# Kernel optimization log

Measured on AMD Instinct MI355X. Metric: run time of the kernel, lower is better.

Reference implementation:

```python
import jax, jax.numpy as jnp
import numpy as np

N = 50000
E = 400000
DIM_IN = 512
DIM_H = 64
HEADS = 8
DIM_OUT = 40
SLOPE = 0.2  # PyG GATv2Conv default negative_slope


def setup_inputs() -> dict:
    key = jax.random.key(0)
    ks = jax.random.split(key, 16)
    s = 0.05
    return {
        "x": jax.random.normal(ks[0], (N, DIM_IN), dtype=jnp.float32),
        "edge_index": jax.random.randint(ks[1], (2, E), 0, N, dtype=jnp.int64),
        "Wl1": jax.random.normal(ks[2], (DIM_IN, HEADS * DIM_H), dtype=jnp.float32) * s,
        "Wr1": jax.random.normal(ks[3], (DIM_IN, HEADS * DIM_H), dtype=jnp.float32) * s,
        "att1": jax.random.normal(ks[4], (HEADS, DIM_H), dtype=jnp.float32) * s,
        "b1": jax.random.normal(ks[5], (HEADS * DIM_H,), dtype=jnp.float32) * s,
        "Wl2": jax.random.normal(ks[6], (HEADS * DIM_H, DIM_OUT), dtype=jnp.float32) * s,
        "Wr2": jax.random.normal(ks[7], (HEADS * DIM_H, DIM_OUT), dtype=jnp.float32) * s,
        "att2": jax.random.normal(ks[8], (1, DIM_OUT), dtype=jnp.float32) * s,
        "b2": jax.random.normal(ks[9], (DIM_OUT,), dtype=jnp.float32) * s,
        "Wl3": jax.random.normal(ks[10], (HEADS * DIM_H, 2), dtype=jnp.float32) * s,
        "Wr3": jax.random.normal(ks[11], (HEADS * DIM_H, 2), dtype=jnp.float32) * s,
        "att3": jax.random.normal(ks[12], (1, 2), dtype=jnp.float32) * s,
        "b3": jax.random.normal(ks[13], (2,), dtype=jnp.float32) * s,
    }


def gatv2(x, src, dst, Wl, Wr, att, b):
    # PyG GATv2Conv: e_ij = att . LeakyReLU(W_l x_j + W_r x_i); softmax over j (by dst i);
    # out_i = sum_j alpha_ij * (W_l x_j); heads concatenated; bias added after.
    n = x.shape[0]
    H, F = att.shape
    xl = (x @ Wl).reshape(n, H, F)  # source transform
    xr = (x @ Wr).reshape(n, H, F)  # target transform
    e = jax.nn.leaky_relu(xl[src] + xr[dst], negative_slope=SLOPE)  # [E, H, F]
    logits = jnp.einsum("ehf,hf->eh", e, att)  # [E, H]
    m = jax.ops.segment_max(logits, dst, num_segments=n)  # self-loops => every segment nonempty
    ex = jnp.exp(logits - m[dst])
    denom = jax.ops.segment_sum(ex, dst, num_segments=n)
    alpha = ex / denom[dst]  # [E, H]
    out = jax.ops.segment_sum(xl[src] * alpha[:, :, None], dst, num_segments=n)  # [N, H, F]
    return out.reshape(n, H * F) + b


def reference(x, edge_index, Wl1, Wr1, att1, b1, Wl2, Wr2, att2, b2, Wl3, Wr3, att3, b3):
    # add self loops (PyG default add_self_loops=True)
    loops = jnp.arange(N, dtype=edge_index.dtype)
    ei = jnp.concatenate([edge_index, jnp.stack([loops, loops])], axis=1)
    src, dst = ei[0], ei[1]
    # eval mode: dropout is identity; ReverseLayerF is identity in forward
    h = jax.nn.relu(gatv2(x, src, dst, Wl1, Wr1, att1, b1))
    y_class = gatv2(h, src, dst, Wl2, Wr2, att2, b2)
    y_domain = gatv2(h, src, dst, Wl3, Wr3, att3, b3)
    return (y_class, y_domain)
```

## Files before the change

kernel.cpp:

```cpp
#include <hip/hip_runtime.h>
#include <math.h>

typedef unsigned short u16;
typedef unsigned int   u32;
typedef __attribute__((ext_vector_type(8))) short bf16x8;
typedef __attribute__((ext_vector_type(4))) float f32x4;
typedef __attribute__((ext_vector_type(4))) u32   u32x4;

__device__ __forceinline__ float b2f(u16 u) {
  union { u32 i; float f; } v; v.i = ((u32)u) << 16; return v.f;
}
__device__ __forceinline__ u16 f2b(float f) {
  union { u32 i; float f; } v; v.f = f;
  u32 r = v.i + 0x7FFFu + ((v.i >> 16) & 1u);
  return (u16)(r >> 16);
}
__device__ __forceinline__ float blo(u32 w) {
  union { u32 i; float f; } v; v.i = w << 16; return v.f;
}
__device__ __forceinline__ float bhi(u32 w) {
  union { u32 i; float f; } v; v.i = w & 0xFFFF0000u; return v.f;
}
__device__ __forceinline__ void ld_lds16(const u16* g, u16* l) {
  __builtin_amdgcn_global_load_lds((const __attribute__((address_space(1))) void*)g,
                                   (__attribute__((address_space(3))) void*)l, 16, 0, 0);
}

#define NN 50000
#define NE 400000
#define NT 450000
#define NBLK_SCAN 196

__global__ void k_detect(const void* x, const void* ei, int* flags) {
  __shared__ int cnt[2];
  int t = threadIdx.x;
  if (t < 2) cnt[t] = 0;
  __syncthreads();
  u16 u = ((const u16*)x)[t];
  int e = (u >> 7) & 0xFF;
  if (u == 0 || (e >= 90 && e <= 134)) atomicAdd(&cnt[0], 1);
  if (t < 16) {
    if (((const int*)ei)[2 * t + 1] == 0) atomicAdd(&cnt[1], 1);
  }
  __syncthreads();
  if (t == 0) {
    flags[0] = (cnt[0] >= 110) ? 1 : 0;
    flags[1] = (cnt[1] >= 15) ? 1 : 0;
  }
}

__device__ __forceinline__ int eidx(const int* ei, int pos, int i64) {
  return i64 ? ei[2 * pos] : ei[pos];
}

__global__ void k_convert_x(const void* x, const int* flags, u16* xb) {
  if (flags[0]) return;
  int c = blockIdx.x * 256 + threadIdx.x;
  const float* xf = (const float*)x + (size_t)c * 8;
  u32x4 o;
  #pragma unroll
  for (int i = 0; i < 4; ++i) {
    u32 lo = f2b(xf[2 * i]);
    u32 hi = f2b(xf[2 * i + 1]);
    o[i] = lo | (hi << 16);
  }
  *(u32x4*)(xb + (size_t)c * 8) = o;
}

__global__ void k_pack_w1t(const void* Wl1, const void* Wr1, const int* flags, u16* w1t) {
  int t = blockIdx.x * 256 + threadIdx.x;
  int k = t >> 10;
  int c = t & 1023;
  const void* W = (c < 512) ? Wl1 : Wr1;
  int cc = c & 511;
  u16 v;
  if (flags[0]) v = ((const u16*)W)[k * 512 + cc];
  else          v = f2b(((const float*)W)[k * 512 + cc]);
  w1t[c * 512 + k] = v;
}

__global__ void k_pack_w23t(const void* Wl2, const void* Wr2, const void* Wl3, const void* Wr3,
                            const int* flags, u16* w23t) {
  int t = blockIdx.x * 256 + threadIdx.x;
  int k = t / 96;
  int c = t % 96;
  const void* W = nullptr; int idx = 0;
  if (c < 40)      { W = Wl2; idx = k * 40 + c; }
  else if (c < 42) { W = Wl3; idx = k * 2 + (c - 40); }
  else if (c < 82) { W = Wr2; idx = k * 40 + (c - 42); }
  else if (c < 84) { W = Wr3; idx = k * 2 + (c - 82); }
  u16 v = 0;
  if (W) {
    if (flags[0]) v = ((const u16*)W)[idx];
    else          v = f2b(((const float*)W)[idx]);
  }
  w23t[c * 512 + k] = v;
}

__global__ void k_pack_params(const void* att1, const void* b1, const void* att2, const void* b2,
                              const void* att3, const void* b3, const int* flags, float* params) {
  int t = blockIdx.x * 256 + threadIdx.x;
  if (t >= 1108) return;
  const void* src; int idx;
  if (t < 512)       { src = att1; idx = t; }
  else if (t < 1024) { src = b1;   idx = t - 512; }
  else if (t < 1064) { src = att2; idx = t - 1024; }
  else if (t < 1104) { src = b2;   idx = t - 1064; }
  else if (t < 1106) { src = att3; idx = t - 1104; }
  else               { src = b3;   idx = t - 1106; }
  params[t] = flags[0] ? b2f(((const u16*)src)[idx]) : ((const float*)src)[idx];
}

__global__ void k_hist(const int* ei, const int* flags, int* deg) {
  int e = blockIdx.x * 256 + threadIdx.x;
  if (e >= NE) return;
  int d = eidx(ei, NE + e, flags[1]);
  atomicAdd(&deg[d], 1);
}

__global__ void k_scanA(const int* deg, int* row_ptr, int* bsum) {
  __shared__ int sh[256];
  int b = blockIdx.x, t = threadIdx.x;
  int i = b * 256 + t;
  int val = (i < NN) ? deg[i] + 1 : 0;
  sh[t] = val;
  __syncthreads();
  #pragma unroll
  for (int off = 1; off < 256; off <<= 1) {
    int v = (t >= off) ? sh[t - off] : 0;
    __syncthreads();
    sh[t] += v;
    __syncthreads();
  }
  if (i < NN) row_ptr[i] = sh[t] - val;
  if (t == 255) bsum[b] = sh[255];
}

__global__ void k_scanB(int* bsum, int* row_ptr) {
  __shared__ int sh[256];
  int t = threadIdx.x;
  int val = (t < NBLK_SCAN) ? bsum[t] : 0;
  sh[t] = val;
  __syncthreads();
  #pragma unroll
  for (int off = 1; off < 256; off <<= 1) {
    int v = (t >= off) ? sh[t - off] : 0;
    __syncthreads();
    sh[t] += v;
    __syncthreads();
  }
  if (t < NBLK_SCAN) bsum[t] = sh[t] - val;
  if (t == 255) row_ptr[NN] = sh[255];
}

__global__ void k_scanC(const int* bsum, int* row_ptr, int* cursor) {
  int i = blockIdx.x * 256 + threadIdx.x;
  if (i < NN) {
    int v = row_ptr[i] + bsum[blockIdx.x];
    row_ptr[i] = v;
    cursor[i] = v;
  }
}

__global__ void k_scatter(const int* ei, const int* flags, int* cursor, int* csr_src) {
  int t = blockIdx.x * 256 + threadIdx.x;
  if (t >= NT) return;
  int i64 = flags[1];
  int s, d;
  if (t < NE) { s = eidx(ei, t, i64); d = eidx(ei, NE + t, i64); }
  else        { s = d = t - NE; }
  int pos = atomicAdd(&cursor[d], 1);
  csr_src[pos] = s;
}

__global__ __launch_bounds__(256) void k_gemm1(const void* __restrict__ xraw, const u16* __restrict__ xb,
                                               const u16* __restrict__ Bt, const int* __restrict__ flags,
                                               u16* __restrict__ XL, u16* __restrict__ XR) {
  __shared__ __align__(16) u16 As[128 * 64];
  __shared__ __align__(16) u16 Bs[128 * 64];
  const int id  = blockIdx.x;
  const int xcd = id & 7;
  const int lb  = id >> 3;
  const int mt  = xcd * 49 + (lb >> 3);
  const int nt  = lb & 7;
  if (mt >= 391) return;
  const int m0 = mt * 128;
  const int n0 = nt * 128;
  const u16* __restrict__ A = flags[0] ? (const u16*)xraw : xb;
  const int t = threadIdx.x;
  const int wave = t >> 6;
  const int lane = t & 63;
  const int wm = (wave >> 1) * 64;
  const int wn = (wave & 1) * 64;
  const int fr = lane & 15;
  const int fk = lane >> 4;
  const int srow = lane >> 3;
  const int schk = (lane & 7) ^ srow;
  f32x4 acc[4][4] = {};
  for (int k0 = 0; k0 < 512; k0 += 64) {
    #pragma unroll
    for (int q = 0; q < 4; ++q) {
      int rbase = wave * 32 + q * 8;
      int gm = m0 + rbase + srow;
      if (gm > NN - 1) gm = NN - 1;
      ld_lds16(&A[(size_t)gm * 512 + k0 + schk * 8], &As[rbase * 64]);
      ld_lds16(&Bt[(size_t)(n0 + rbase + srow) * 512 + k0 + schk * 8], &Bs[rbase * 64]);
    }
    __syncthreads();
    #pragma unroll
    for (int h = 0; h < 2; ++h) {
      int s = h * 4 + fk;
      bf16x8 af[4], bb[4];
      #pragma unroll
      for (int i = 0; i < 4; ++i) {
        int row = wm + i * 16 + fr;
        af[i] = *(const bf16x8*)&As[row * 64 + ((s ^ (row & 7)) * 8)];
      }
      #pragma unroll
      for (int j = 0; j < 4; ++j) {
        int row = wn + j * 16 + fr;
        bb[j] = *(const bf16x8*)&Bs[row * 64 + ((s ^ (row & 7)) * 8)];
      }
      #pragma unroll
      for (int i = 0; i < 4; ++i)
        #pragma unroll
        for (int j = 0; j < 4; ++j)
          acc[i][j] = __builtin_amdgcn_mfma_f32_16x16x32_bf16(af[i], bb[j], acc[i][j], 0, 0, 0);
    }
    __syncthreads();
  }
  #pragma unroll
  for (int i = 0; i < 4; ++i) {
    #pragma unroll
    for (int r = 0; r < 4; ++r) {
      int gm = m0 + wm + i * 16 + fk * 4 + r;
      if (gm < NN) {
        #pragma unroll
        for (int j = 0; j < 4; ++j) {
          int gn = n0 + wn + j * 16 + fr;
          u16 v = f2b(acc[i][j][r]);
          if (gn < 512) XL[(size_t)gm * 512 + gn] = v;
          else          XR[(size_t)gm * 512 + gn - 512] = v;
        }
      }
    }
  }
}

__global__ __launch_bounds__(256) void k_gemm2(const u16* __restrict__ A, const u16* __restrict__ Bt,
                                               float* __restrict__ C) {
  __shared__ __align__(16) short As[128][40];
  __shared__ __align__(16) short Bs[96][40];
  const int m0 = blockIdx.x * 128;
  const int t = threadIdx.x;
  const int wave = t >> 6;
  const int lane = t & 63;
  const int fr = lane & 15;
  const int fk = lane >> 4;
  const int wm = wave * 32;
  f32x4 acc[2][6] = {};
  for (int k0 = 0; k0 < 512; k0 += 32) {
    #pragma unroll
    for (int h = 0; h < 2; ++h) {
      int c = t + h * 256;
      int row = c >> 2, kc = (c & 3) * 8;
      int gm = m0 + row;
      u32x4 va = {0, 0, 0, 0};
      if (gm < NN) va = *(const u32x4*)&A[(size_t)gm * 512 + k0 + kc];
      *(u32x4*)&As[row][kc] = va;
    }
    for (int c = t; c < 384; c += 256) {
      int row = c >> 2, kc = (c & 3) * 8;
      *(u32x4*)&Bs[row][kc] = *(const u32x4*)&Bt[row * 512 + k0 + kc];
    }
    __syncthreads();
    bf16x8 af[2], bb[6];
    #pragma unroll
    for (int i = 0; i < 2; ++i) af[i] = *(const bf16x8*)&As[wm + i * 16 + fr][fk * 8];
    #pragma unroll
    for (int j = 0; j < 6; ++j) bb[j] = *(const bf16x8*)&Bs[j * 16 + fr][fk * 8];
    #pragma unroll
    for (int i = 0; i < 2; ++i)
      #pragma unroll
      for (int j = 0; j < 6; ++j)
        acc[i][j] = __builtin_amdgcn_mfma_f32_16x16x32_bf16(af[i], bb[j], acc[i][j], 0, 0, 0);
    __syncthreads();
  }
  #pragma unroll
  for (int i = 0; i < 2; ++i) {
    #pragma unroll
    for (int j = 0; j < 6; ++j) {
      int gn = j * 16 + fr;
      if (gn < 84) {
        #pragma unroll
        for (int r = 0; r < 4; ++r) {
          int gm = m0 + wm + i * 16 + fk * 4 + r;
          if (gm < NN) C[(size_t)gm * 84 + gn] = acc[i][j][r];
        }
      }
    }
  }
}

__global__ __launch_bounds__(256) void k_layer1f(const u16* __restrict__ xl1, const u16* __restrict__ xr1,
                                                 const int* __restrict__ row_ptr, const int* __restrict__ csr_src,
                                                 const float* __restrict__ params, u16* __restrict__ hb) {
  int wid = blockIdx.x * 4 + (threadIdx.x >> 6);
  int lane = threadIdx.x & 63;
  int nw = gridDim.x * 4;
  float att[8];
  #pragma unroll
  for (int k = 0; k < 8; ++k) att[k] = params[lane * 8 + k];
  for (int i = wid; i < NN; i += nw) {
    int e0 = row_ptr[i], e1 = row_ptr[i + 1];
    u32x4 xrv = *(const u32x4*)&xr1[(size_t)i * 512 + lane * 8];
    float xr[8];
    #pragma unroll
    for (int q = 0; q < 4; ++q) { xr[2 * q] = blo(xrv[q]); xr[2 * q + 1] = bhi(xrv[q]); }
    float s = 0.f;
    float acc[8] = {0.f, 0.f, 0.f, 0.f, 0.f, 0.f, 0.f, 0.f};
    int q0 = csr_src[e0];
    int q1 = csr_src[e0 + 1 < e1 ? e0 + 1 : e1 - 1];
    int q2 = csr_src[e0 + 2 < e1 ? e0 + 2 : e1 - 1];
    int q3 = csr_src[e0 + 3 < e1 ? e0 + 3 : e1 - 1];
    for (int p = e0; p < e1; p += 4) {
      int j0 = q0, j1 = q1, j2 = q2, j3 = q3;
      u32x4 v0 = *(const u32x4*)&xl1[(size_t)j0 * 512 + lane * 8];
      u32x4 v1 = *(const u32x4*)&xl1[(size_t)j1 * 512 + lane * 8];
      u32x4 v2 = *(const u32x4*)&xl1[(size_t)j2 * 512 + lane * 8];
      u32x4 v3 = *(const u32x4*)&xl1[(size_t)j3 * 512 + lane * 8];
      int np = p + 4;
      if (np < e1) {
        q0 = csr_src[np];
        q1 = csr_src[np + 1 < e1 ? np + 1 : e1 - 1];
        q2 = csr_src[np + 2 < e1 ? np + 2 : e1 - 1];
        q3 = csr_src[np + 3 < e1 ? np + 3 : e1 - 1];
      }
      float m1 = (p + 1 < e1) ? 1.f : 0.f;
      float m2 = (p + 2 < e1) ? 1.f : 0.f;
      float m3 = (p + 3 < e1) ? 1.f : 0.f;
      float c0 = 0.f, c1 = 0.f, c2 = 0.f, c3 = 0.f;
      float xlv0[8], xlv1[8], xlv2[8], xlv3[8];
      #pragma unroll
      for (int q = 0; q < 4; ++q) {
        xlv0[2 * q] = blo(v0[q]); xlv0[2 * q + 1] = bhi(v0[q]);
        xlv1[2 * q] = blo(v1[q]); xlv1[2 * q + 1] = bhi(v1[q]);
        xlv2[2 * q] = blo(v2[q]); xlv2[2 * q + 1] = bhi(v2[q]);
        xlv3[2 * q] = blo(v3[q]); xlv3[2 * q + 1] = bhi(v3[q]);
      }
      #pragma unroll
      for (int k = 0; k < 8; ++k) {
        float t0 = xlv0[k] + xr[k];
        float t1 = xlv1[k] + xr[k];
        float t2 = xlv2[k] + xr[k];
        float t3 = xlv3[k] + xr[k];
        c0 = fmaf(att[k], fmaxf(t0, 0.2f * t0), c0);
        c1 = fmaf(att[k], fmaxf(t1, 0.2f * t1), c1);
        c2 = fmaf(att[k], fmaxf(t2, 0.2f * t2), c2);
        c3 = fmaf(att[k], fmaxf(t3, 0.2f * t3), c3);
      }
      c0 += __shfl_xor(c0, 1, 64); c1 += __shfl_xor(c1, 1, 64);
      c2 += __shfl_xor(c2, 1, 64); c3 += __shfl_xor(c3, 1, 64);
      c0 += __shfl_xor(c0, 2, 64); c1 += __shfl_xor(c1, 2, 64);
      c2 += __shfl_xor(c2, 2, 64); c3 += __shfl_xor(c3, 2, 64);
      c0 += __shfl_xor(c0, 4, 64); c1 += __shfl_xor(c1, 4, 64);
      c2 += __shfl_xor(c2, 4, 64); c3 += __shfl_xor(c3, 4, 64);
      float pv0 = __expf(fminf(fmaxf(c0, -30.f), 30.f));
      float pv1 = __expf(fminf(fmaxf(c1, -30.f), 30.f)) * m1;
      float pv2 = __expf(fminf(fmaxf(c2, -30.f), 30.f)) * m2;
      float pv3 = __expf(fminf(fmaxf(c3, -30.f), 30.f)) * m3;
      s += (pv0 + pv1) + (pv2 + pv3);
      #pragma unroll
      for (int k = 0; k < 8; ++k) {
        float a = fmaf(pv0, xlv0[k], pv1 * xlv1[k]);
        float b = fmaf(pv2, xlv2[k], pv3 * xlv3[k]);
        acc[k] += a + b;
      }
    }
    float r = 1.f / s;
    u32x4 o;
    #pragma unroll
    for (int q = 0; q < 4; ++q) {
      u32 lo = f2b(fmaxf(fmaf(acc[2 * q],     r, params[512 + lane * 8 + 2 * q]),     0.f));
      u32 hi = f2b(fmaxf(fmaf(acc[2 * q + 1], r, params[512 + lane * 8 + 2 * q + 1]), 0.f));
      o[q] = lo | (hi << 16);
    }
    *(u32x4*)&hb[(size_t)i * 512 + lane * 8] = o;
  }
}

__global__ __launch_bounds__(256) void k_layer23f(const float* __restrict__ xlr23, const int* __restrict__ row_ptr,
                                                  const int* __restrict__ csr_src, const float* __restrict__ params,
                                                  const int* __restrict__ flags, void* __restrict__ out) {
  int wid = blockIdx.x * 4 + (threadIdx.x >> 6);
  int lane = threadIdx.x & 63;
  int nw = gridDim.x * 4;
  int c = lane;
  bool act = c < 42;
  float att = 0.f;
  if (c < 40)      att = params[1024 + c];
  else if (c < 42) att = params[1104 + (c - 40)];
  int isbf = flags[0];
  for (int i = wid; i < NN; i += nw) {
    int e0 = row_ptr[i], e1 = row_ptr[i + 1];
    float xr = act ? xlr23[(size_t)i * 84 + 42 + c] : 0.f;
    float s2 = 0.f, s3 = 0.f, acc = 0.f;
    for (int p = e0; p < e1; p += 2) {
      int p1 = p + 1 < e1 ? p + 1 : e1 - 1;
      float m1 = (p + 1 < e1) ? 1.f : 0.f;
      int j0 = csr_src[p], j1 = csr_src[p1];
      float xl0 = act ? xlr23[(size_t)j0 * 84 + c] : 0.f;
      float xl1 = act ? xlr23[(size_t)j1 * 84 + c] : 0.f;
      float t0 = xl0 + xr, t1 = xl1 + xr;
      float v0 = att * fmaxf(t0, 0.2f * t0);
      float v1 = att * fmaxf(t1, 0.2f * t1);
      float w0 = (c < 40) ? v0 : 0.f;
      float w1 = (c < 40) ? v1 : 0.f;
      #pragma unroll
      for (int o = 32; o >= 1; o >>= 1) { w0 += __shfl_xor(w0, o, 64); w1 += __shfl_xor(w1, o, 64); }
      float u0 = v0 + __shfl_xor(v0, 1, 64);
      float u1 = v1 + __shfl_xor(v1, 1, 64);
      float l3_0 = __shfl(u0, 40, 64);
      float l3_1 = __shfl(u1, 40, 64);
      float p2_0 = __expf(fminf(fmaxf(w0, -30.f), 30.f));
      float p2_1 = __expf(fminf(fmaxf(w1, -30.f), 30.f)) * m1;
      float p3_0 = __expf(fminf(fmaxf(l3_0, -30.f), 30.f));
      float p3_1 = __expf(fminf(fmaxf(l3_1, -30.f), 30.f)) * m1;
      s2 += p2_0 + p2_1;
      s3 += p3_0 + p3_1;
      float a0 = (c < 40) ? p2_0 : p3_0;
      float a1 = (c < 40) ? p2_1 : p3_1;
      acc += fmaf(a0, xl0, a1 * xl1);
    }
    if (c < 40) {
      float v = acc / s2 + params[1064 + c];
      size_t o = (size_t)i * 40 + c;
      if (isbf) ((u16*)out)[o] = f2b(v); else ((float*)out)[o] = v;
    } else if (c < 42) {
      float v = acc / s3 + params[1106 + (c - 40)];
      size_t o = 2000000 + (size_t)i * 2 + (c - 40);
      if (isbf) ((u16*)out)[o] = f2b(v); else ((float*)out)[o] = v;
    }
  }
}

extern "C" void kernel_launch(void* const* d_in, const int* in_sizes, int n_in,
                              void* d_out, int out_size, void* d_ws, size_t ws_size,
                              hipStream_t stream) {
  const void* x    = d_in[0];
  const int*  ei   = (const int*)d_in[1];
  const void* Wl1  = d_in[2];
  const void* Wr1  = d_in[3];
  const void* att1 = d_in[4];
  const void* b1   = d_in[5];
  const void* Wl2  = d_in[6];
  const void* Wr2  = d_in[7];
  const void* att2 = d_in[8];
  const void* b2   = d_in[9];
  const void* Wl3  = d_in[10];
  const void* Wr3  = d_in[11];
  const void* att3 = d_in[12];
  const void* b3   = d_in[13];
  (void)in_sizes; (void)n_in; (void)out_size;

  char* ws = (char*)d_ws;
  size_t off = 0;
  auto alloc = [&](size_t bytes) -> void* {
    void* p = ws + off;
    off = (off + bytes + 255) & ~(size_t)255;
    return p;
  };
  int*   flags   = (int*)  alloc(64);
  u16*   xb      = (u16*)  alloc((size_t)NN * 512 * 2);
  u16*   w1t     = (u16*)  alloc((size_t)1024 * 512 * 2);
  u16*   xl1     = (u16*)  alloc((size_t)NN * 512 * 2);
  u16*   xr1     = (u16*)  alloc((size_t)NN * 512 * 2);
  u16*   hb      = (u16*)  alloc((size_t)NN * 512 * 2);
  u16*   w23t    = (u16*)  alloc((size_t)96 * 512 * 2);
  float* xlr23   = (float*)alloc((size_t)NN * 84 * 4);
  float* params  = (float*)alloc(1108 * 4);
  int*   row_ptr = (int*)  alloc((NN + 1) * 4);
  int*   deg     = (int*)  alloc(NN * 4);
  int*   cursor  = (int*)  alloc(NN * 4);
  int*   csr_src = (int*)  alloc((NT + 16) * 4);
  int*   bsum    = (int*)  alloc(256 * 4);
  if (ws_size < off) return;

  hipLaunchKernelGGL(k_detect, dim3(1), dim3(128), 0, stream, x, (const void*)ei, flags);
  hipLaunchKernelGGL(k_convert_x, dim3(12500), dim3(256), 0, stream, x, flags, xb);
  hipLaunchKernelGGL(k_pack_w1t, dim3(2048), dim3(256), 0, stream, Wl1, Wr1, flags, w1t);
  hipLaunchKernelGGL(k_pack_w23t, dim3(192), dim3(256), 0, stream, Wl2, Wr2, Wl3, Wr3, flags, w23t);
  hipLaunchKernelGGL(k_pack_params, dim3(5), dim3(256), 0, stream, att1, b1, att2, b2, att3, b3, flags, params);
  hipMemsetAsync(deg, 0, NN * 4, stream);
  hipLaunchKernelGGL(k_hist, dim3((NE + 255) / 256), dim3(256), 0, stream, ei, flags, deg);
  hipLaunchKernelGGL(k_scanA, dim3(NBLK_SCAN), dim3(256), 0, stream, deg, row_ptr, bsum);
  hipLaunchKernelGGL(k_scanB, dim3(1), dim3(256), 0, stream, bsum, row_ptr);
  hipLaunchKernelGGL(k_scanC, dim3(NBLK_SCAN), dim3(256), 0, stream, bsum, row_ptr, cursor);
  hipLaunchKernelGGL(k_scatter, dim3((NT + 255) / 256), dim3(256), 0, stream, ei, flags, cursor, csr_src);
  hipLaunchKernelGGL(k_gemm1, dim3(3136), dim3(256), 0, stream, x, xb, w1t, flags, xl1, xr1);
  hipLaunchKernelGGL(k_layer1f, dim3(4096), dim3(256), 0, stream, xl1, xr1, row_ptr, csr_src, params, hb);
  hipLaunchKernelGGL(k_gemm2, dim3(391), dim3(256), 0, stream, hb, w23t, xlr23);
  hipLaunchKernelGGL(k_layer23f, dim3(4096), dim3(256), 0, stream, xlr23, row_ptr, csr_src, params, flags, d_out);
}
```

Before: 471.8 us.

## Split LeakyReLU into linear plus abs term, precompute linear dots in GEMM epilogue

Rewrites LeakyReLU(t) as 0.6*t + 0.4*|t|, so the linear part of the attention logit becomes per-node dot products (att·xl_j and att·xr_i). The GEMM1 epilogue computes these per head and stores them in dotL/dotR. The edge loop then only needs fabs plus an FMA per element, and it adds the two precomputed scalars. The aggregation sums are also restructured into FMA chains. This trades a cheaper per-edge inner loop for an extra gathered scalar load per edge, extra epilogue shuffles in GEMM1, and bf16 rounding differences because the dot is taken from fp32 accumulators.

```diff
diff --git a/kernel.cpp b/kernel.cpp
--- a/kernel.cpp
+++ b/kernel.cpp
@@ -175,7 +175,9 @@
 
 __global__ __launch_bounds__(256) void k_gemm1(const void* __restrict__ xraw, const u16* __restrict__ xb,
                                                const u16* __restrict__ Bt, const int* __restrict__ flags,
-                                               u16* __restrict__ XL, u16* __restrict__ XR) {
+                                               const float* __restrict__ params,
+                                               u16* __restrict__ XL, u16* __restrict__ XR,
+                                               float* __restrict__ dotL, float* __restrict__ dotR) {
   __shared__ __align__(16) u16 As[128 * 64];
   __shared__ __align__(16) u16 Bs[128 * 64];
   const int id  = blockIdx.x;
@@ -229,6 +231,31 @@
     }
     __syncthreads();
   }
+  {
+    const int cb = (n0 + wn) & 511;
+    const bool isL = (n0 + wn) < 512;
+    const int hd = cb >> 6;
+    float* __restrict__ dvec = isL ? dotL : dotR;
+    float attv[4];
+    #pragma unroll
+    for (int j = 0; j < 4; ++j) attv[j] = params[cb + j * 16 + fr];
+    #pragma unroll
+    for (int i = 0; i < 4; ++i) {
+      #pragma unroll
+      for (int r = 0; r < 4; ++r) {
+        float d = attv[0] * acc[i][0][r];
+        d = fmaf(attv[1], acc[i][1][r], d);
+        d = fmaf(attv[2], acc[i][2][r], d);
+        d = fmaf(attv[3], acc[i][3][r], d);
+        d += __shfl_xor(d, 1, 64);
+        d += __shfl_xor(d, 2, 64);
+        d += __shfl_xor(d, 4, 64);
+        d += __shfl_xor(d, 8, 64);
+        int gm = m0 + wm + i * 16 + fk * 4 + r;
+        if (fr == 0 && gm < NN) dvec[(size_t)gm * 8 + hd] = 0.6f * d;
+      }
+    }
+  }
   #pragma unroll
   for (int i = 0; i < 4; ++i) {
     #pragma unroll
@@ -303,17 +330,20 @@
 }
 
 __global__ __launch_bounds__(256) void k_layer1f(const u16* __restrict__ xl1, const u16* __restrict__ xr1,
+                                                 const float* __restrict__ dotL, const float* __restrict__ dotR,
                                                  const int* __restrict__ row_ptr, const int* __restrict__ csr_src,
                                                  const float* __restrict__ params, u16* __restrict__ hb) {
   int wid = blockIdx.x * 4 + (threadIdx.x >> 6);
   int lane = threadIdx.x & 63;
   int nw = gridDim.x * 4;
+  int grp = lane >> 3;
   float att[8];
   #pragma unroll
-  for (int k = 0; k < 8; ++k) att[k] = params[lane * 8 + k];
+  for (int k = 0; k < 8; ++k) att[k] = 0.4f * params[lane * 8 + k];
   for (int i = wid; i < NN; i += nw) {
     int e0 = row_ptr[i], e1 = row_ptr[i + 1];
     u32x4 xrv = *(const u32x4*)&xr1[(size_t)i * 512 + lane * 8];
+    float dRi = dotR[(size_t)i * 8 + grp];
     float xr[8];
     #pragma unroll
     for (int q = 0; q < 4; ++q) { xr[2 * q] = blo(xrv[q]); xr[2 * q + 1] = bhi(xrv[q]); }
@@ -329,6 +359,10 @@
       u32x4 v1 = *(const u32x4*)&xl1[(size_t)j1 * 512 + lane * 8];
       u32x4 v2 = *(const u32x4*)&xl1[(size_t)j2 * 512 + lane * 8];
       u32x4 v3 = *(const u32x4*)&xl1[(size_t)j3 * 512 + lane * 8];
+      float dl0 = dotL[(size_t)j0 * 8 + grp];
+      float dl1 = dotL[(size_t)j1 * 8 + grp];
+      float dl2 = dotL[(size_t)j2 * 8 + grp];
+      float dl3 = dotL[(size_t)j3 * 8 + grp];
       int np = p + 4;
       if (np < e1) {
         q0 = csr_src[np];
@@ -354,10 +388,10 @@
         float t1 = xlv1[k] + xr[k];
         float t2 = xlv2[k] + xr[k];
         float t3 = xlv3[k] + xr[k];
-        c0 = fmaf(att[k], fmaxf(t0, 0.2f * t0), c0);
-        c1 = fmaf(att[k], fmaxf(t1, 0.2f * t1), c1);
-        c2 = fmaf(att[k], fmaxf(t2, 0.2f * t2), c2);
-        c3 = fmaf(att[k], fmaxf(t3, 0.2f * t3), c3);
+        c0 = fmaf(att[k], fabsf(t0), c0);
+        c1 = fmaf(att[k], fabsf(t1), c1);
+        c2 = fmaf(att[k], fabsf(t2), c2);
+        c3 = fmaf(att[k], fabsf(t3), c3);
       }
       c0 += __shfl_xor(c0, 1, 64); c1 += __shfl_xor(c1, 1, 64);
       c2 += __shfl_xor(c2, 1, 64); c3 += __shfl_xor(c3, 1, 64);
@@ -365,16 +399,21 @@
       c2 += __shfl_xor(c2, 2, 64); c3 += __shfl_xor(c3, 2, 64);
       c0 += __shfl_xor(c0, 4, 64); c1 += __shfl_xor(c1, 4, 64);
       c2 += __shfl_xor(c2, 4, 64); c3 += __shfl_xor(c3, 4, 64);
-      float pv0 = __expf(fminf(fmaxf(c0, -30.f), 30.f));
-      float pv1 = __expf(fminf(fmaxf(c1, -30.f), 30.f)) * m1;
-      float pv2 = __expf(fminf(fmaxf(c2, -30.f), 30.f)) * m2;
-      float pv3 = __expf(fminf(fmaxf(c3, -30.f), 30.f)) * m3;
+      float l0 = c0 + dl0 + dRi;
+      float l1 = c1 + dl1 + dRi;
+      float l2 = c2 + dl2 + dRi;
+      float l3 = c3 + dl3 + dRi;
+      float pv0 = __expf(fminf(fmaxf(l0, -30.f), 30.f));
+      float pv1 = __expf(fminf(fmaxf(l1, -30.f), 30.f)) * m1;
+      float pv2 = __expf(fminf(fmaxf(l2, -30.f), 30.f)) * m2;
+      float pv3 = __expf(fminf(fmaxf(l3, -30.f), 30.f)) * m3;
       s += (pv0 + pv1) + (pv2 + pv3);
       #pragma unroll
       for (int k = 0; k < 8; ++k) {
-        float a = fmaf(pv0, xlv0[k], pv1 * xlv1[k]);
-        float b = fmaf(pv2, xlv2[k], pv3 * xlv3[k]);
-        acc[k] += a + b;
+        float a = fmaf(pv0, xlv0[k], acc[k]);
+        a = fmaf(pv1, xlv1[k], a);
+        a = fmaf(pv2, xlv2[k], a);
+        acc[k] = fmaf(pv3, xlv3[k], a);
       }
     }
     float r = 1.f / s;
@@ -430,7 +469,7 @@
       s3 += p3_0 + p3_1;
       float a0 = (c < 40) ? p2_0 : p3_0;
       float a1 = (c < 40) ? p2_1 : p3_1;
-      acc += fmaf(a0, xl0, a1 * xl1);
+      acc = fmaf(a1, xl1, fmaf(a0, xl0, acc));
     }
     if (c < 40) {
       float v = acc / s2 + params[1064 + c];
@@ -479,6 +518,8 @@
   u16*   w23t    = (u16*)  alloc((size_t)96 * 512 * 2);
   float* xlr23   = (float*)alloc((size_t)NN * 84 * 4);
   float* params  = (float*)alloc(1108 * 4);
+  float* dotL    = (float*)alloc((size_t)NN * 8 * 4);
+  float* dotR    = (float*)alloc((size_t)NN * 8 * 4);
   int*   row_ptr = (int*)  alloc((NN + 1) * 4);
   int*   deg     = (int*)  alloc(NN * 4);
   int*   cursor  = (int*)  alloc(NN * 4);
@@ -497,8 +538,8 @@
   hipLaunchKernelGGL(k_scanB, dim3(1), dim3(256), 0, stream, bsum, row_ptr);
   hipLaunchKernelGGL(k_scanC, dim3(NBLK_SCAN), dim3(256), 0, stream, bsum, row_ptr, cursor);
   hipLaunchKernelGGL(k_scatter, dim3((NT + 255) / 256), dim3(256), 0, stream, ei, flags, cursor, csr_src);
-  hipLaunchKernelGGL(k_gemm1, dim3(3136), dim3(256), 0, stream, x, xb, w1t, flags, xl1, xr1);
-  hipLaunchKernelGGL(k_layer1f, dim3(4096), dim3(256), 0, stream, xl1, xr1, row_ptr, csr_src, params, hb);
+  hipLaunchKernelGGL(k_gemm1, dim3(3136), dim3(256), 0, stream, x, xb, w1t, flags, params, xl1, xr1, dotL, dotR);
+  hipLaunchKernelGGL(k_layer1f, dim3(4096), dim3(256), 0, stream, xl1, xr1, dotL, dotR, row_ptr, csr_src, params, hb);
   hipLaunchKernelGGL(k_gemm2, dim3(391), dim3(256), 0, stream, hb, w23t, xlr23);
   hipLaunchKernelGGL(k_layer23f, dim3(4096), dim3(256), 0, stream, xlr23, row_ptr, csr_src, params, flags, d_out);
 }
```

Result: slower. 507.2 us (+7.5%).
